# Performance work log

Measured on AMD Instinct MI355X. Metric: run time of the kernel, lower is better.

The kernel has to match this reference:

```python
import jax, jax.numpy as jnp
import numpy as np

N_GRAPH = 100000
N_CAND = 10
N_TOTAL = N_GRAPH + N_CAND
F_IN = 128
N_TYPES = 10
E = 6400000


def _p(key, shape, scale=0.05):
    return scale * jax.random.normal(key, shape, dtype=jnp.float32)


def setup_inputs() -> dict:
    key = jax.random.key(0)
    ks = jax.random.split(key, 20)
    x = jax.random.normal(ks[0], (N_GRAPH, F_IN), dtype=jnp.float32)
    candidate_set = jax.random.normal(ks[1], (N_CAND, F_IN), dtype=jnp.float32)
    edge_index = jax.random.randint(ks[2], (2, E), 0, N_GRAPH, dtype=jnp.int64)
    candidate_idx = jnp.arange(N_GRAPH, N_TOTAL, dtype=jnp.int64)  # candidate nodes appended last
    return {
        "x": x, "candidate_set": candidate_set,
        "edge_index": edge_index, "candidate_idx": candidate_idx,
        "W1": _p(ks[3], (F_IN, 16)), "b1": jnp.zeros((16,), jnp.float32),
        "W2": _p(ks[4], (16, 24)), "b2": jnp.zeros((24,), jnp.float32),
        "W3": _p(ks[5], (24, 32)), "b3": jnp.zeros((32,), jnp.float32),
        "Ws1": _p(ks[6], (32, 16)), "bs1": jnp.zeros((16,), jnp.float32),
        "Ws2": _p(ks[7], (16, N_TYPES)), "bs2": jnp.zeros((N_TYPES,), jnp.float32),
        "We1": _p(ks[8], (32, 24)), "be1": jnp.zeros((24,), jnp.float32),
        "We2": _p(ks[9], (24, N_TYPES)), "be2": jnp.zeros((N_TYPES,), jnp.float32),
    }


def _gcn(h, src, dst, W, b, n):
    # GCNConv: x' = D^{-1/2}(A+I)D^{-1/2} X W + b (self-loops added)
    h = h @ W
    deg = jax.ops.segment_sum(jnp.ones(src.shape, h.dtype), dst, num_segments=n) + 1.0
    dinv = jax.lax.rsqrt(deg)
    msg = h[src] * (dinv[src] * dinv[dst])[:, None]
    out = jax.ops.segment_sum(msg, dst, num_segments=n)
    out = out + h * (dinv * dinv)[:, None]  # self-loop term
    return out + b


def relu6(x):
    return jnp.clip(x, 0.0, 6.0)


def reference(x, candidate_set, edge_index, candidate_idx,
              W1, b1, W2, b2, W3, b3,
              Ws1, bs1, Ws2, bs2, We1, be1, We2, be2):
    n = N_TOTAL
    src, dst = edge_index[0], edge_index[1]
    h = jnp.concatenate([x, candidate_set], axis=0)  # [n, F_IN]
    h = _gcn(h, src, dst, W1, b1, n)
    h = _gcn(h, src, dst, W2, b2, n)
    h = _gcn(h, src, dst, W3, b3, n)  # [n, 32]

    start_probs = jax.nn.softmax(relu6(h @ Ws1 + bs1) @ Ws2 + bs2, axis=0)  # [n, T]
    mask = jnp.ones_like(start_probs).at[candidate_idx].set(0.0)
    start_probs = start_probs * mask
    start_probs = jnp.where(start_probs == 0.0, 1e-10, start_probs)
    k1, k2 = jax.random.split(jax.random.key(42))
    start_node = jax.random.categorical(k1, jnp.log(start_probs), axis=-1)  # [n]

    combined = jnp.concatenate([h, h[start_node]], axis=0)  # [2n, 32]
    end_probs = jax.nn.softmax(relu6(combined @ We1 + be1) @ We2 + be2, axis=0)  # [2n, T]
    end_probs = end_probs.at[start_node].set(0.0)
    end_probs = jnp.where(end_probs == 0.0, 1e-10, end_probs)
    end_node = jax.random.categorical(k2, jnp.log(end_probs), axis=-1)  # [2n]
    return (start_node, end_node, start_probs, end_probs)
```

## Files before the change

### kernel.cpp

```cpp
#include <hip/hip_runtime.h>
#include <stdint.h>

constexpr int N_GRAPH = 100000;
constexpr int N_CANDS = 10;
constexpr int NT      = N_GRAPH + N_CANDS;
constexpr int F_IN    = 128;
constexpr int NTYPES  = 10;
constexpr int NE      = 6400000;

constexpr int CB_SHIFT = 9;
constexpr int CB       = 1 << CB_SHIFT;
constexpr int NBK2     = (NT + CB - 1) / CB;
constexpr int SB       = 512;
constexpr int NMAT     = NBK2 * SB;
constexpr int NSCAN_B  = NMAT / 256;
constexpr int TMPENT_CAP = NE + NMAT * 15 + 16;

#define RNG_VARIANT 0

typedef float f4v __attribute__((ext_vector_type(4)));

__device__ __forceinline__ void tf2x32(uint32_t k0, uint32_t k1, uint32_t x0, uint32_t x1,
                                       uint32_t& o0, uint32_t& o1) {
  const uint32_t ks2 = k0 ^ k1 ^ 0x1BD11BDAu;
  uint32_t v0 = x0 + k0, v1 = x1 + k1;
#define TFR(r) { v0 += v1; v1 = (v1 << (r)) | (v1 >> (32 - (r))); v1 ^= v0; }
  TFR(13) TFR(15) TFR(26) TFR(6)
  v0 += k1;  v1 += ks2 + 1u;
  TFR(17) TFR(29) TFR(16) TFR(24)
  v0 += ks2; v1 += k0 + 2u;
  TFR(13) TFR(15) TFR(26) TFR(6)
  v0 += k0;  v1 += k1 + 3u;
  TFR(17) TFR(29) TFR(16) TFR(24)
  v0 += k1;  v1 += ks2 + 4u;
  TFR(13) TFR(15) TFR(26) TFR(6)
  v0 += ks2; v1 += k0 + 5u;
#undef TFR
  o0 = v0; o1 = v1;
}

__device__ __forceinline__ void derive_keys(uint32_t& a0, uint32_t& a1,
                                            uint32_t& b0, uint32_t& b1) {
#if RNG_VARIANT == 2
  uint32_t c0, c1, d0, d1;
  tf2x32(0u, 42u, 0u, 2u, c0, c1);
  tf2x32(0u, 42u, 1u, 3u, d0, d1);
  a0 = c0; a1 = d0; b0 = c1; b1 = d1;
#else
  tf2x32(0u, 42u, 0u, 0u, a0, a1);
  tf2x32(0u, 42u, 0u, 1u, b0, b1);
#endif
}

__device__ __forceinline__ uint32_t rng_bits(uint32_t k0, uint32_t k1,
                                             uint32_t idx, uint32_t total) {
#if RNG_VARIANT == 0
  uint32_t o0, o1; tf2x32(k0, k1, 0u, idx, o0, o1); return o0 ^ o1;
#elif RNG_VARIANT == 1
  uint32_t o0, o1; tf2x32(k0, k1, 0u, idx, o0, o1); return o1;
#else
  uint32_t half = total >> 1; uint32_t o0, o1;
  if (idx < half) { tf2x32(k0, k1, idx, idx + half, o0, o1); return o0; }
  tf2x32(k0, k1, idx - half, idx, o0, o1); return o1;
#endif
}

__device__ __forceinline__ double gumbel_from_bits(uint32_t bits) {
  float uf = __uint_as_float((bits >> 9) | 0x3f800000u) - 1.0f;
  uf = fmaxf(1.17549435e-38f, uf + 1.17549435e-38f);
  return -log(-log((double)uf));
}

__device__ __forceinline__ uint32_t encf(float f) {
  uint32_t u = __float_as_uint(f);
  return u ^ ((u & 0x80000000u) ? 0xFFFFFFFFu : 0x80000000u);
}
__device__ __forceinline__ float decf(uint32_t e) {
  uint32_t u = (e & 0x80000000u) ? (e ^ 0x80000000u) : ~e;
  return __uint_as_float(u);
}

__global__ __launch_bounds__(512) void k_bcount(const int* __restrict__ dst,
                                                int* __restrict__ cntmat,
                                                int* __restrict__ cnt) {
  __shared__ int h[NBK2];
  int tid = threadIdx.x, blk = blockIdx.x;
  for (int b = tid; b < NBK2; b += 512) h[b] = 0;
  __syncthreads();
  int per = (NE + SB - 1) / SB;
  int e0 = blk * per, e1 = min(e0 + per, NE);
  for (int e = e0 + tid; e < e1; e += 512) atomicAdd(&h[dst[e] >> CB_SHIFT], 1);
  __syncthreads();
  for (int b = tid; b < NBK2; b += 512) {
    int c = h[b];
    cntmat[b * SB + blk] = (c + 15) & ~15;
    if (c) atomicAdd(&cnt[b], c);
  }
}

__global__ __launch_bounds__(256) void k_s1(int* __restrict__ cmat, int* __restrict__ partial) {
  __shared__ int sm[256];
  int t = blockIdx.x * 256 + threadIdx.x;
  int v = cmat[t];
  sm[threadIdx.x] = v;
  __syncthreads();
  #pragma unroll
  for (int s = 1; s < 256; s <<= 1) {
    int a = (threadIdx.x >= s) ? sm[threadIdx.x - s] : 0;
    __syncthreads();
    sm[threadIdx.x] += a;
    __syncthreads();
  }
  cmat[t] = sm[threadIdx.x] - v;
  if (threadIdx.x == 255) partial[blockIdx.x] = sm[255];
}

__global__ __launch_bounds__(512) void k_s2(int* __restrict__ partial, int* __restrict__ cmat) {
  __shared__ int sm[512];
  int t = threadIdx.x;
  int v = (t < NSCAN_B) ? partial[t] : 0;
  sm[t] = v;
  __syncthreads();
  #pragma unroll
  for (int s = 1; s < 512; s <<= 1) {
    int a = (t >= s) ? sm[t - s] : 0;
    __syncthreads();
    sm[t] += a;
    __syncthreads();
  }
  if (t < NSCAN_B) partial[t] = sm[t] - v;
  if (t == 511) cmat[NMAT] = sm[511];
}

__global__ __launch_bounds__(256) void k_s3(int* __restrict__ cmat, const int* __restrict__ partial) {
  int t = blockIdx.x * 256 + threadIdx.x;
  cmat[t] += partial[blockIdx.x];
}

__global__ __launch_bounds__(256) void k_rowscan(const int* __restrict__ cnt,
                                                 int* __restrict__ rowbase) {
  __shared__ int sm[256];
  int t = threadIdx.x;
  int v = (t < NBK2) ? cnt[t] : 0;
  sm[t] = v;
  __syncthreads();
  #pragma unroll
  for (int s = 1; s < 256; s <<= 1) {
    int a = (t >= s) ? sm[t - s] : 0;
    __syncthreads();
    sm[t] += a;
    __syncthreads();
  }
  if (t < NBK2) rowbase[t] = sm[t] - v;
}

__global__ __launch_bounds__(512) void k_scatter2(const int* __restrict__ src,
                                                  const int* __restrict__ dst,
                                                  const int* __restrict__ cmat,
                                                  uint32_t* __restrict__ tmpent) {
  __shared__ int lcur[NBK2];
  int tid = threadIdx.x, blk = blockIdx.x;
  for (int b = tid; b < NBK2; b += 512) lcur[b] = cmat[b * SB + blk];
  __syncthreads();
  int per = (NE + SB - 1) / SB;
  int e0 = blk * per, e1 = min(e0 + per, NE);
  for (int e = e0 + tid; e < e1; e += 512) {
    int s = src[e], d = dst[e];
    int b = d >> CB_SHIFT;
    int pos = atomicAdd(&lcur[b], 1);
    tmpent[pos] = (uint32_t)s | ((uint32_t)(d & (CB - 1)) << 17);
  }
  __syncthreads();
  for (int b = tid; b < NBK2; b += 512) {
    int p = lcur[b];
    int end = cmat[b * SB + blk + 1];
    for (; p < end; ++p) tmpent[p] = 0xFFFFFFFFu;
  }
}

__global__ __launch_bounds__(512) void k_place(const uint32_t* __restrict__ tmpent,
                                               const int* __restrict__ cmat,
                                               const int* __restrict__ rowbase,
                                               int* __restrict__ rowptr,
                                               float* __restrict__ dinv,
                                               int* __restrict__ col) {
  __shared__ int sdeg[CB];
  __shared__ int sexc[CB];
  __shared__ int sscan[CB];
  int b = blockIdx.x, tid = threadIdx.x;
  sdeg[tid] = 0;
  __syncthreads();
  int r0 = cmat[b * SB], r1 = cmat[(b + 1) * SB];
  for (int e = r0 + tid; e < r1; e += 512) {
    uint32_t v = tmpent[e];
    if (v != 0xFFFFFFFFu) atomicAdd(&sdeg[v >> 17], 1);
  }
  __syncthreads();
  int d = sdeg[tid];
  sscan[tid] = d;
  __syncthreads();
  #pragma unroll
  for (int s = 1; s < CB; s <<= 1) {
    int v = (tid >= s) ? sscan[tid - s] : 0;
    __syncthreads();
    sscan[tid] += v;
    __syncthreads();
  }
  int rb = rowbase[b];
  int incl = rb + sscan[tid];
  sexc[tid] = incl - d;
  int i = b * CB + tid;
  if (i < NT) {
    rowptr[i + 1] = incl;
    dinv[i] = (float)(1.0 / sqrt((double)(d + 1)));
  }
  if (b == 0 && tid == 0) rowptr[0] = 0;
  __syncthreads();
  for (int e = r0 + tid; e < r1; e += 512) {
    uint32_t v = tmpent[e];
    if (v != 0xFFFFFFFFu) {
      int pos = atomicAdd(&sexc[v >> 17], 1);
      col[pos] = (int)(v & 0x1FFFFu);
    }
  }
}

__global__ __launch_bounds__(256) void k_mm1(const float* __restrict__ x, const float* __restrict__ cand,
                                             const float* __restrict__ W, const float* __restrict__ dinv,
                                             float* __restrict__ zs0) {
  int gid = blockIdx.x * 256 + threadIdx.x;
  if (gid >= NT * 4) return;
  int i = gid >> 2, f4 = gid & 3;
  const float* hr = (i < N_GRAPH) ? (x + (size_t)i * F_IN)
                                  : (cand + (size_t)(i - N_GRAPH) * F_IN);
  const float4* h4 = reinterpret_cast<const float4*>(hr);
  const float4* W4 = reinterpret_cast<const float4*>(W);
  double a0 = 0.0, a1 = 0.0, a2 = 0.0, a3 = 0.0;
  #pragma unroll 8
  for (int q = 0; q < 32; ++q) {
    float4 hv = h4[q];
    float4 w0 = W4[(4 * q + 0) * 4 + f4];
    float4 w1 = W4[(4 * q + 1) * 4 + f4];
    float4 w2 = W4[(4 * q + 2) * 4 + f4];
    float4 w3 = W4[(4 * q + 3) * 4 + f4];
    a0 += (double)hv.x * w0.x + (double)hv.y * w1.x + (double)hv.z * w2.x + (double)hv.w * w3.x;
    a1 += (double)hv.x * w0.y + (double)hv.y * w1.y + (double)hv.z * w2.y + (double)hv.w * w3.y;
    a2 += (double)hv.x * w0.z + (double)hv.y * w1.z + (double)hv.z * w2.z + (double)hv.w * w3.z;
    a3 += (double)hv.x * w0.w + (double)hv.y * w1.w + (double)hv.z * w2.w + (double)hv.w * w3.w;
  }
  double di = (double)dinv[i];
  float4 o;
  o.x = (float)(a0 * di); o.y = (float)(a1 * di);
  o.z = (float)(a2 * di); o.w = (float)(a3 * di);
  reinterpret_cast<float4*>(zs0)[(size_t)i * 4 + f4] = o;
}

template <bool SQ, bool WITHW, int R>
__global__ __launch_bounds__(8 * R) void k_prop3(const int* __restrict__ rowptr,
                                                 const int* __restrict__ col,
                                                 const float* __restrict__ zin,
                                                 const float* __restrict__ win,
                                                 const float* __restrict__ dinv,
                                                 float* __restrict__ zout,
                                                 float* __restrict__ wout,
                                                 float* __restrict__ wsout) {
  int i = blockIdx.x * R + threadIdx.y;
  if (i >= NT) return;
  int fx = threadIdx.x & 3;
  int es = threadIdx.x >> 2;
  const float4* z4 = reinterpret_cast<const float4*>(zin);
  int e0 = rowptr[i], e1 = rowptr[i + 1];
  int ngrp = (e1 - e0) >> 2;
  double a0 = 0.0, a1 = 0.0, a2 = 0.0, a3 = 0.0, wa = 0.0;
  const bool dow = WITHW && (fx == 0);
  for (int gq = es; gq < ngrp; gq += 2) {
    int e = e0 + (gq << 2);
    int c0 = __builtin_nontemporal_load(col + e);
    int c1 = __builtin_nontemporal_load(col + e + 1);
    int c2 = __builtin_nontemporal_load(col + e + 2);
    int c3 = __builtin_nontemporal_load(col + e + 3);
    float4 v0 = z4[(size_t)c0 * 4 + fx];
    float4 v1 = z4[(size_t)c1 * 4 + fx];
    float4 v2 = z4[(size_t)c2 * 4 + fx];
    float4 v3 = z4[(size_t)c3 * 4 + fx];
    if (dow)
      wa += (double)win[c0] + (double)win[c1] + (double)win[c2] + (double)win[c3];
    a0 += (double)v0.x + (double)v1.x + (double)v2.x + (double)v3.x;
    a1 += (double)v0.y + (double)v1.y + (double)v2.y + (double)v3.y;
    a2 += (double)v0.z + (double)v1.z + (double)v2.z + (double)v3.z;
    a3 += (double)v0.w + (double)v1.w + (double)v2.w + (double)v3.w;
  }
  if (es == (ngrp & 1)) {
    for (int e = e0 + (ngrp << 2); e < e1; ++e) {
      int c = __builtin_nontemporal_load(col + e);
      float4 v = z4[(size_t)c * 4 + fx];
      if (dow) wa += (double)win[c];
      a0 += (double)v.x; a1 += (double)v.y; a2 += (double)v.z; a3 += (double)v.w;
    }
  }
  a0 += __shfl_xor(a0, 4);
  a1 += __shfl_xor(a1, 4);
  a2 += __shfl_xor(a2, 4);
  a3 += __shfl_xor(a3, 4);
  if (WITHW) wa += __shfl_xor(wa, 4);
  if (es == 0) {
    float4 s = z4[(size_t)i * 4 + fx];
    a0 += (double)s.x; a1 += (double)s.y; a2 += (double)s.z; a3 += (double)s.w;
    double di = (double)dinv[i];
    double sc = SQ ? di * di : di;
    float4 o;
    o.x = (float)(sc * a0); o.y = (float)(sc * a1);
    o.z = (float)(sc * a2); o.w = (float)(sc * a3);
    reinterpret_cast<float4*>(zout)[(size_t)i * 4 + fx] = o;
    if (dow) {
      wa += (double)win[i];
      double w = di * wa;
      wout[i]  = (float)w;
      wsout[i] = (float)(di * w);
    }
  }
}

__global__ __launch_bounds__(512) void k_small(const float* __restrict__ W2, const float* __restrict__ b2p,
                                               const float* __restrict__ W3, const float* __restrict__ b1p,
                                               double* __restrict__ M, double* __restrict__ u,
                                               double* __restrict__ v) {
  __shared__ double t[24];
  int tid = threadIdx.x;
  if (tid < 24) {
    double a = 0.0;
    for (int k = 0; k < 16; ++k) a += (double)b1p[k] * (double)W2[k * 24 + tid];
    t[tid] = a;
  }
  if (tid >= 32 && tid < 64) {
    int o = tid - 32;
    double a = 0.0;
    for (int j = 0; j < 24; ++j) a += (double)b2p[j] * (double)W3[j * 32 + o];
    v[o] = a;
  }
  __syncthreads();
  if (tid < 32) {
    double a = 0.0;
    for (int j = 0; j < 24; ++j) a += t[j] * (double)W3[j * 32 + tid];
    u[tid] = a;
  }
  {
    int k = tid >> 5, o = tid & 31;
    double a = 0.0;
    for (int j = 0; j < 24; ++j) a += (double)W2[k * 24 + j] * (double)W3[j * 32 + o];
    M[tid] = a;
  }
}

__global__ __launch_bounds__(256) void k_epi(const float* __restrict__ z3, const float* __restrict__ w1,
                                             const float* __restrict__ w2,
                                             const double* __restrict__ M, const double* __restrict__ u,
                                             const double* __restrict__ v, const float* __restrict__ b3,
                                             float* __restrict__ H) {
  int gid = blockIdx.x * 256 + threadIdx.x;
  if (gid >= NT * 32) return;
  int i = gid >> 5, o = gid & 31;
  const float* zr = z3 + (size_t)i * 16;
  double acc = (double)b3[o] + (double)w2[i] * u[o] + (double)w1[i] * v[o];
  #pragma unroll
  for (int k = 0; k < 16; ++k) acc += (double)zr[k] * M[k * 32 + o];
  H[gid] = (float)acc;
}

template <int HID>
__global__ __launch_bounds__(256) void k_head(const float* __restrict__ H, const int* __restrict__ sn,
                                              int nrows,
                                              const float* __restrict__ Wa, const float* __restrict__ ba,
                                              const float* __restrict__ Wb, const float* __restrict__ bb,
                                              float* __restrict__ logits) {
  int i = blockIdx.x * 256 + threadIdx.x;
  if (i >= nrows) return;
  int row = (i < NT) ? i : sn[i - NT];
  const float* hr = H + (size_t)row * 32;
  float h[32];
  #pragma unroll
  for (int k = 0; k < 32; ++k) h[k] = hr[k];
  double hid[HID];
  for (int j = 0; j < HID; ++j) {
    double a = (double)ba[j];
    #pragma unroll
    for (int k = 0; k < 32; ++k) a += (double)h[k] * (double)Wa[k * HID + j];
    hid[j] = fmin(fmax(a, 0.0), 6.0);
  }
  for (int t = 0; t < NTYPES; ++t) {
    double l = (double)bb[t];
    #pragma unroll
    for (int j = 0; j < HID; ++j) l += hid[j] * (double)Wb[j * NTYPES + t];
    logits[(size_t)i * NTYPES + t] = (float)l;
  }
}

__global__ __launch_bounds__(256) void k_colmax(const float* __restrict__ L, int nrows,
                                                uint32_t* __restrict__ mb) {
  __shared__ float sm[256][NTYPES];
  float m[NTYPES];
  #pragma unroll
  for (int t = 0; t < NTYPES; ++t) m[t] = -3.402823466e38f;
  for (int r = blockIdx.x * 256 + threadIdx.x; r < nrows; r += gridDim.x * 256) {
    #pragma unroll
    for (int t = 0; t < NTYPES; ++t) m[t] = fmaxf(m[t], L[(size_t)r * NTYPES + t]);
  }
  #pragma unroll
  for (int t = 0; t < NTYPES; ++t) sm[threadIdx.x][t] = m[t];
  __syncthreads();
  for (int s = 128; s > 0; s >>= 1) {
    if (threadIdx.x < s)
      for (int t = 0; t < NTYPES; ++t)
        sm[threadIdx.x][t] = fmaxf(sm[threadIdx.x][t], sm[threadIdx.x + s][t]);
    __syncthreads();
  }
  if (threadIdx.x < NTYPES) atomicMax(&mb[threadIdx.x], encf(sm[0][threadIdx.x]));
}

__global__ __launch_bounds__(256) void k_colsum(const float* __restrict__ L, int nrows,
                                                const uint32_t* __restrict__ mb,
                                                double* __restrict__ sums) {
  __shared__ double sm[256][NTYPES];
  float mx[NTYPES];
  #pragma unroll
  for (int t = 0; t < NTYPES; ++t) mx[t] = decf(mb[t]);
  double s[NTYPES];
  #pragma unroll
  for (int t = 0; t < NTYPES; ++t) s[t] = 0.0;
  for (int r = blockIdx.x * 256 + threadIdx.x; r < nrows; r += gridDim.x * 256) {
    #pragma unroll
    for (int t = 0; t < NTYPES; ++t)
      s[t] += exp((double)L[(size_t)r * NTYPES + t] - (double)mx[t]);
  }
  #pragma unroll
  for (int t = 0; t < NTYPES; ++t) sm[threadIdx.x][t] = s[t];
  __syncthreads();
  for (int st = 128; st > 0; st >>= 1) {
    if (threadIdx.x < st)
      for (int t = 0; t < NTYPES; ++t)
        sm[threadIdx.x][t] += sm[threadIdx.x + st][t];
    __syncthreads();
  }
  if (threadIdx.x < NTYPES) atomicAdd(&sums[threadIdx.x], sm[0][threadIdx.x]);
}

__global__ __launch_bounds__(256) void k_ps_start(const float* __restrict__ L,
                                                  const uint32_t* __restrict__ mb,
                                                  const double* __restrict__ sums,
                                                  float* __restrict__ P,
                                                  float* __restrict__ outSN,
                                                  int* __restrict__ sn,
                                                  int* __restrict__ flags) {
  int i = blockIdx.x * 256 + threadIdx.x;
  if (i >= NT) return;
  uint32_t a0, a1, b0, b1; derive_keys(a0, a1, b0, b1);
  double best = -1e300; int bi = 0;
  #pragma unroll
  for (int t = 0; t < NTYPES; ++t) {
    double p = exp((double)L[(size_t)i * NTYPES + t] - (double)decf(mb[t])) / sums[t];
    float pf = (float)p;
    if (i >= N_GRAPH || pf == 0.0f) pf = 1e-10f;
    P[(size_t)i * NTYPES + t] = pf;
    uint32_t bits = rng_bits(a0, a1, (uint32_t)(i * NTYPES + t), (uint32_t)(NT * NTYPES));
    double v = log((double)pf) + gumbel_from_bits(bits);
    if (v > best) { best = v; bi = t; }
  }
  sn[i] = bi;
  outSN[i] = (float)bi;
  flags[bi] = 1;
}

__global__ __launch_bounds__(256) void k_ps_end(const float* __restrict__ L,
                                                const uint32_t* __restrict__ mb,
                                                const double* __restrict__ sums,
                                                const int* __restrict__ flags,
                                                float* __restrict__ P,
                                                float* __restrict__ outEN) {
  int j = blockIdx.x * 256 + threadIdx.x;
  if (j >= 2 * NT) return;
  uint32_t a0, a1, b0, b1; derive_keys(a0, a1, b0, b1);
  const bool rowmask = (j < NTYPES && flags[j]);
  double best = -1e300; int bi = 0;
  #pragma unroll
  for (int t = 0; t < NTYPES; ++t) {
    double p = exp((double)L[(size_t)j * NTYPES + t] - (double)decf(mb[t])) / sums[t];
    float pf = (float)p;
    if (rowmask || pf == 0.0f) pf = 1e-10f;
    P[(size_t)j * NTYPES + t] = pf;
    uint32_t bits = rng_bits(b0, b1, (uint32_t)(j * NTYPES + t), (uint32_t)(2 * NT * NTYPES));
    double v = log((double)pf) + gumbel_from_bits(bits);
    if (v > best) { best = v; bi = t; }
  }
  outEN[j] = (float)bi;
}

extern "C" void kernel_launch(void* const* d_in, const int* in_sizes, int n_in,
                              void* d_out, int out_size, void* d_ws, size_t ws_size,
                              hipStream_t stream) {
  const float* x    = (const float*)d_in[0];
  const float* cand = (const float*)d_in[1];
  const int*   ei   = (const int*)d_in[2];
  const float* W1 = (const float*)d_in[4];  const float* b1 = (const float*)d_in[5];
  const float* W2 = (const float*)d_in[6];  const float* b2 = (const float*)d_in[7];
  const float* W3 = (const float*)d_in[8];  const float* b3 = (const float*)d_in[9];
  const float* Ws1 = (const float*)d_in[10]; const float* bs1 = (const float*)d_in[11];
  const float* Ws2 = (const float*)d_in[12]; const float* bs2 = (const float*)d_in[13];
  const float* We1 = (const float*)d_in[14]; const float* be1 = (const float*)d_in[15];
  const float* We2 = (const float*)d_in[16]; const float* be2 = (const float*)d_in[17];
  float* out = (float*)d_out;
  float* outSN = out;
  float* outEN = out + NT;
  float* outPS = out + 3 * NT;
  float* outPE = out + 13 * NT;

  char* ws = (char*)d_ws;
  size_t off = 0;
  auto alloc = [&](size_t bytes) -> void* {
    void* p = ws + off;
    off += (bytes + 511) & ~(size_t)511;
    return p;
  };
  float*    dinv    = (float*)alloc((size_t)NT * 4);
  int*      rowptr  = (int*)alloc((size_t)(NT + 1) * 4);
  int*      cnt     = (int*)alloc((size_t)NBK2 * 4);
  int*      rowbase = (int*)alloc((size_t)NBK2 * 4);
  int*      cmat    = (int*)alloc((size_t)(NMAT + 1) * 4);
  int*      partial = (int*)alloc(512 * 4);
  int*      col     = (int*)alloc((size_t)NE * 4);
  char*     ublk    = (char*)alloc((size_t)TMPENT_CAP * 4);
  uint32_t* tmpent  = (uint32_t*)ublk;
  float*    zsA     = (float*)ublk;
  float*    zsB     = (float*)(ublk + (size_t)NT * 16 * 4);
  float*    Ha      = (float*)(ublk + (size_t)NT * 16 * 4 * 2);
  float*    logitsS = (float*)alloc((size_t)NT * NTYPES * 4);
  float*    logitsE = (float*)alloc((size_t)2 * NT * NTYPES * 4);
  float*    w1v     = (float*)alloc((size_t)NT * 4);
  float*    ws1v    = (float*)alloc((size_t)NT * 4);
  float*    w2v     = (float*)alloc((size_t)NT * 4);
  float*    wsd     = (float*)alloc((size_t)NT * 4);
  double*   Md      = (double*)alloc(512 * 8);
  double*   ud      = (double*)alloc(32 * 8);
  double*   vd      = (double*)alloc(32 * 8);
  int*      sn      = (int*)alloc((size_t)NT * 4);
  uint32_t* maxS    = (uint32_t*)alloc(64);
  double*   sumS    = (double*)alloc(128);
  uint32_t* maxE    = (uint32_t*)alloc(64);
  double*   sumE    = (double*)alloc(128);
  int*      flags   = (int*)alloc(64);
  (void)ws_size; (void)in_sizes; (void)n_in; (void)out_size;

  const int* srcA = ei;
  const int* dstA = ei + NE;

  const int B = 256;
  auto blocks = [](long long nthreads) { return (int)((nthreads + 255) / 256); };

  hipMemsetAsync(cnt, 0, (size_t)NBK2 * 4, stream);
  k_bcount<<<SB, 512, 0, stream>>>(dstA, cmat, cnt);
  k_s1<<<NSCAN_B, 256, 0, stream>>>(cmat, partial);
  k_s2<<<1, 512, 0, stream>>>(partial, cmat);
  k_s3<<<NSCAN_B, 256, 0, stream>>>(cmat, partial);
  k_rowscan<<<1, 256, 0, stream>>>(cnt, rowbase);
  k_scatter2<<<SB, 512, 0, stream>>>(srcA, dstA, cmat, tmpent);
  k_place<<<NBK2, 512, 0, stream>>>(tmpent, cmat, rowbase, rowptr, dinv, col);

  k_small<<<1, 512, 0, stream>>>(W2, b2, W3, b1, Md, ud, vd);
  k_mm1<<<blocks((long long)NT * 4), B, 0, stream>>>(x, cand, W1, dinv, zsA);
  const int PR3 = 32, PBLK = (NT + PR3 - 1) / PR3;
  k_prop3<true,  true,  PR3><<<PBLK, dim3(8, PR3), 0, stream>>>(rowptr, col, zsA, dinv, dinv, zsB, w1v, ws1v);
  k_prop3<true,  true,  PR3><<<PBLK, dim3(8, PR3), 0, stream>>>(rowptr, col, zsB, ws1v, dinv, zsA, w2v, wsd);
  k_prop3<false, false, PR3><<<PBLK, dim3(8, PR3), 0, stream>>>(rowptr, col, zsA, nullptr, dinv, zsB, nullptr, nullptr);
  k_epi<<<blocks((long long)NT * 32), B, 0, stream>>>(zsB, w1v, w2v, Md, ud, vd, b3, Ha);

  k_head<16><<<blocks(NT), B, 0, stream>>>(Ha, sn, NT, Ws1, bs1, Ws2, bs2, logitsS);
  hipMemsetAsync(maxS, 0, (size_t)((char*)flags - (char*)maxS) + 512, stream);
  k_colmax<<<512, B, 0, stream>>>(logitsS, NT, maxS);
  k_colsum<<<512, B, 0, stream>>>(logitsS, NT, maxS, sumS);
  k_ps_start<<<blocks(NT), B, 0, stream>>>(logitsS, maxS, sumS, outPS, outSN, sn, flags);

  k_head<24><<<blocks(2 * NT), B, 0, stream>>>(Ha, sn, 2 * NT, We1, be1, We2, be2, logitsE);
  k_colmax<<<512, B, 0, stream>>>(logitsE, 2 * NT, maxE);
  k_colsum<<<512, B, 0, stream>>>(logitsE, 2 * NT, maxE, sumE);
  k_ps_end<<<blocks((long long)2 * NT), B, 0, stream>>>(logitsE, maxE, sumE, flags, outPE, outEN);
}
```

Baseline: 787.5 us.

## Split SpMM gather into two source-half passes for L2 locality

Each row's CSR neighbours are partitioned by whether the source index falls in the lower or upper half of nodes, and each propagation layer runs as two passes, one per half. Partial sums from the first pass go to a double-precision scratch buffer that the second pass reads back and finishes. The aim is that each pass gathers from a feature table half the size, so it fits better in cache and random gathers hit more often. The gather loop is also unrolled to issue eight loads per iteration. In exchange there are extra kernel launches, partial-sum writes and reads, and more shared atomics in CSR placement.

```diff
diff --git a/kernel.cpp b/kernel.cpp
--- a/kernel.cpp
+++ b/kernel.cpp
@@ -16,9 +16,12 @@
 constexpr int NSCAN_B  = NMAT / 256;
 constexpr int TMPENT_CAP = NE + NMAT * 15 + 16;
 
+constexpr int HSPLIT = NT / 2;
+
 #define RNG_VARIANT 0
 
-typedef float f4v __attribute__((ext_vector_type(4)));
+typedef float  f4v __attribute__((ext_vector_type(4)));
+typedef double d2v __attribute__((ext_vector_type(2)));
 
 __device__ __forceinline__ void tf2x32(uint32_t k0, uint32_t k1, uint32_t x0, uint32_t x1,
                                        uint32_t& o0, uint32_t& o1) {
@@ -182,18 +185,26 @@
                                                const int* __restrict__ cmat,
                                                const int* __restrict__ rowbase,
                                                int* __restrict__ rowptr,
+                                               int* __restrict__ rowmid,
                                                float* __restrict__ dinv,
                                                int* __restrict__ col) {
   __shared__ int sdeg[CB];
-  __shared__ int sexc[CB];
+  __shared__ int sdlo[CB];
   __shared__ int sscan[CB];
+  __shared__ int sclo[CB];
+  __shared__ int schi[CB];
   int b = blockIdx.x, tid = threadIdx.x;
   sdeg[tid] = 0;
+  sdlo[tid] = 0;
   __syncthreads();
   int r0 = cmat[b * SB], r1 = cmat[(b + 1) * SB];
   for (int e = r0 + tid; e < r1; e += 512) {
     uint32_t v = tmpent[e];
-    if (v != 0xFFFFFFFFu) atomicAdd(&sdeg[v >> 17], 1);
+    if (v != 0xFFFFFFFFu) {
+      int d = v >> 17;
+      atomicAdd(&sdeg[d], 1);
+      if ((int)(v & 0x1FFFFu) < HSPLIT) atomicAdd(&sdlo[d], 1);
+    }
   }
   __syncthreads();
   int d = sdeg[tid];
@@ -208,10 +219,14 @@
   }
   int rb = rowbase[b];
   int incl = rb + sscan[tid];
-  sexc[tid] = incl - d;
+  int exc  = incl - d;
+  int mid  = exc + sdlo[tid];
+  sclo[tid] = exc;
+  schi[tid] = mid;
   int i = b * CB + tid;
   if (i < NT) {
     rowptr[i + 1] = incl;
+    rowmid[i] = mid;
     dinv[i] = (float)(1.0 / sqrt((double)(d + 1)));
   }
   if (b == 0 && tid == 0) rowptr[0] = 0;
@@ -219,8 +234,10 @@
   for (int e = r0 + tid; e < r1; e += 512) {
     uint32_t v = tmpent[e];
     if (v != 0xFFFFFFFFu) {
-      int pos = atomicAdd(&sexc[v >> 17], 1);
-      col[pos] = (int)(v & 0x1FFFFu);
+      int dd = v >> 17;
+      int s = (int)(v & 0x1FFFFu);
+      int pos = (s < HSPLIT) ? atomicAdd(&sclo[dd], 1) : atomicAdd(&schi[dd], 1);
+      col[pos] = s;
     }
   }
 }
@@ -255,12 +272,15 @@
   reinterpret_cast<float4*>(zs0)[(size_t)i * 4 + f4] = o;
 }
 
-template <bool SQ, bool WITHW, int R>
-__global__ __launch_bounds__(8 * R) void k_prop3(const int* __restrict__ rowptr,
+template <bool SQ, bool WITHW, int PASS, int R>
+__global__ __launch_bounds__(8 * R) void k_prop4(const int* __restrict__ rowptr,
+                                                 const int* __restrict__ rowmid,
                                                  const int* __restrict__ col,
                                                  const float* __restrict__ zin,
                                                  const float* __restrict__ win,
                                                  const float* __restrict__ dinv,
+                                                 double* __restrict__ zpart,
+                                                 double* __restrict__ wpart,
                                                  float* __restrict__ zout,
                                                  float* __restrict__ wout,
                                                  float* __restrict__ wsout) {
@@ -269,11 +289,46 @@
   int fx = threadIdx.x & 3;
   int es = threadIdx.x >> 2;
   const float4* z4 = reinterpret_cast<const float4*>(zin);
-  int e0 = rowptr[i], e1 = rowptr[i + 1];
+  int e0, e1;
+  if (PASS == 0) { e0 = rowptr[i]; e1 = rowmid[i]; }
+  else           { e0 = rowmid[i]; e1 = rowptr[i + 1]; }
   int ngrp = (e1 - e0) >> 2;
   double a0 = 0.0, a1 = 0.0, a2 = 0.0, a3 = 0.0, wa = 0.0;
   const bool dow = WITHW && (fx == 0);
-  for (int gq = es; gq < ngrp; gq += 2) {
+  int gq = es;
+  for (; gq + 4 <= ngrp; gq += 4) {
+    int ea = e0 + (gq << 2);
+    int eb = e0 + ((gq + 2) << 2);
+    int c0 = __builtin_nontemporal_load(col + ea);
+    int c1 = __builtin_nontemporal_load(col + ea + 1);
+    int c2 = __builtin_nontemporal_load(col + ea + 2);
+    int c3 = __builtin_nontemporal_load(col + ea + 3);
+    int c4 = __builtin_nontemporal_load(col + eb);
+    int c5 = __builtin_nontemporal_load(col + eb + 1);
+    int c6 = __builtin_nontemporal_load(col + eb + 2);
+    int c7 = __builtin_nontemporal_load(col + eb + 3);
+    float4 v0 = z4[(size_t)c0 * 4 + fx];
+    float4 v1 = z4[(size_t)c1 * 4 + fx];
+    float4 v2 = z4[(size_t)c2 * 4 + fx];
+    float4 v3 = z4[(size_t)c3 * 4 + fx];
+    float4 v4 = z4[(size_t)c4 * 4 + fx];
+    float4 v5 = z4[(size_t)c5 * 4 + fx];
+    float4 v6 = z4[(size_t)c6 * 4 + fx];
+    float4 v7 = z4[(size_t)c7 * 4 + fx];
+    if (dow) {
+      wa += (double)win[c0] + (double)win[c1] + (double)win[c2] + (double)win[c3];
+      wa += (double)win[c4] + (double)win[c5] + (double)win[c6] + (double)win[c7];
+    }
+    a0 += (double)v0.x + (double)v1.x + (double)v2.x + (double)v3.x;
+    a1 += (double)v0.y + (double)v1.y + (double)v2.y + (double)v3.y;
+    a2 += (double)v0.z + (double)v1.z + (double)v2.z + (double)v3.z;
+    a3 += (double)v0.w + (double)v1.w + (double)v2.w + (double)v3.w;
+    a0 += (double)v4.x + (double)v5.x + (double)v6.x + (double)v7.x;
+    a1 += (double)v4.y + (double)v5.y + (double)v6.y + (double)v7.y;
+    a2 += (double)v4.z + (double)v5.z + (double)v6.z + (double)v7.z;
+    a3 += (double)v4.w + (double)v5.w + (double)v6.w + (double)v7.w;
+  }
+  for (; gq < ngrp; gq += 2) {
     int e = e0 + (gq << 2);
     int c0 = __builtin_nontemporal_load(col + e);
     int c1 = __builtin_nontemporal_load(col + e + 1);
@@ -304,19 +359,32 @@
   a3 += __shfl_xor(a3, 4);
   if (WITHW) wa += __shfl_xor(wa, 4);
   if (es == 0) {
-    float4 s = z4[(size_t)i * 4 + fx];
-    a0 += (double)s.x; a1 += (double)s.y; a2 += (double)s.z; a3 += (double)s.w;
-    double di = (double)dinv[i];
-    double sc = SQ ? di * di : di;
-    float4 o;
-    o.x = (float)(sc * a0); o.y = (float)(sc * a1);
-    o.z = (float)(sc * a2); o.w = (float)(sc * a3);
-    reinterpret_cast<float4*>(zout)[(size_t)i * 4 + fx] = o;
-    if (dow) {
-      wa += (double)win[i];
-      double w = di * wa;
-      wout[i]  = (float)w;
-      wsout[i] = (float)(di * w);
+    d2v* zp = reinterpret_cast<d2v*>(zpart) + (size_t)i * 8 + fx * 2;
+    if (PASS == 0) {
+      d2v p0; p0.x = a0; p0.y = a1;
+      d2v p1; p1.x = a2; p1.y = a3;
+      __builtin_nontemporal_store(p0, zp);
+      __builtin_nontemporal_store(p1, zp + 1);
+      if (dow) wpart[i] = wa;
+    } else {
+      d2v q0 = __builtin_nontemporal_load(zp);
+      d2v q1 = __builtin_nontemporal_load(zp + 1);
+      a0 += q0.x; a1 += q0.y; a2 += q1.x; a3 += q1.y;
+      float4 s = z4[(size_t)i * 4 + fx];
+      a0 += (double)s.x; a1 += (double)s.y; a2 += (double)s.z; a3 += (double)s.w;
+      double di = (double)dinv[i];
+      double sc = SQ ? di * di : di;
+      f4v o;
+      o.x = (float)(sc * a0); o.y = (float)(sc * a1);
+      o.z = (float)(sc * a2); o.w = (float)(sc * a3);
+      __builtin_nontemporal_store(o, reinterpret_cast<f4v*>(zout) + (size_t)i * 4 + fx);
+      if (dow) {
+        wa += wpart[i];
+        wa += (double)win[i];
+        double w = di * wa;
+        wout[i]  = (float)w;
+        wsout[i] = (float)(di * w);
+      }
     }
   }
 }
@@ -522,6 +590,7 @@
   };
   float*    dinv    = (float*)alloc((size_t)NT * 4);
   int*      rowptr  = (int*)alloc((size_t)(NT + 1) * 4);
+  int*      rowmid  = (int*)alloc((size_t)NT * 4);
   int*      cnt     = (int*)alloc((size_t)NBK2 * 4);
   int*      rowbase = (int*)alloc((size_t)NBK2 * 4);
   int*      cmat    = (int*)alloc((size_t)(NMAT + 1) * 4);
@@ -532,6 +601,8 @@
   float*    zsA     = (float*)ublk;
   float*    zsB     = (float*)(ublk + (size_t)NT * 16 * 4);
   float*    Ha      = (float*)(ublk + (size_t)NT * 16 * 4 * 2);
+  double*   zpart   = (double*)Ha;
+  double*   wpart   = (double*)(ublk + (size_t)NT * 16 * 4 * 4);
   float*    logitsS = (float*)alloc((size_t)NT * NTYPES * 4);
   float*    logitsE = (float*)alloc((size_t)2 * NT * NTYPES * 4);
   float*    w1v     = (float*)alloc((size_t)NT * 4);
@@ -562,14 +633,18 @@
   k_s3<<<NSCAN_B, 256, 0, stream>>>(cmat, partial);
   k_rowscan<<<1, 256, 0, stream>>>(cnt, rowbase);
   k_scatter2<<<SB, 512, 0, stream>>>(srcA, dstA, cmat, tmpent);
-  k_place<<<NBK2, 512, 0, stream>>>(tmpent, cmat, rowbase, rowptr, dinv, col);
+  k_place<<<NBK2, 512, 0, stream>>>(tmpent, cmat, rowbase, rowptr, rowmid, dinv, col);
 
   k_small<<<1, 512, 0, stream>>>(W2, b2, W3, b1, Md, ud, vd);
   k_mm1<<<blocks((long long)NT * 4), B, 0, stream>>>(x, cand, W1, dinv, zsA);
   const int PR3 = 32, PBLK = (NT + PR3 - 1) / PR3;
-  k_prop3<true,  true,  PR3><<<PBLK, dim3(8, PR3), 0, stream>>>(rowptr, col, zsA, dinv, dinv, zsB, w1v, ws1v);
-  k_prop3<true,  true,  PR3><<<PBLK, dim3(8, PR3), 0, stream>>>(rowptr, col, zsB, ws1v, dinv, zsA, w2v, wsd);
-  k_prop3<false, false, PR3><<<PBLK, dim3(8, PR3), 0, stream>>>(rowptr, col, zsA, nullptr, dinv, zsB, nullptr, nullptr);
+  dim3 pdim(8, PR3);
+  k_prop4<true,  true,  0, PR3><<<PBLK, pdim, 0, stream>>>(rowptr, rowmid, col, zsA, dinv, dinv, zpart, wpart, nullptr, nullptr, nullptr);
+  k_prop4<true,  true,  1, PR3><<<PBLK, pdim, 0, stream>>>(rowptr, rowmid, col, zsA, dinv, dinv, zpart, wpart, zsB, w1v, ws1v);
+  k_prop4<true,  true,  0, PR3><<<PBLK, pdim, 0, stream>>>(rowptr, rowmid, col, zsB, ws1v, dinv, zpart, wpart, nullptr, nullptr, nullptr);
+  k_prop4<true,  true,  1, PR3><<<PBLK, pdim, 0, stream>>>(rowptr, rowmid, col, zsB, ws1v, dinv, zpart, wpart, zsA, w2v, wsd);
+  k_prop4<false, false, 0, PR3><<<PBLK, pdim, 0, stream>>>(rowptr, rowmid, col, zsA, nullptr, dinv, zpart, wpart, nullptr, nullptr, nullptr);
+  k_prop4<false, false, 1, PR3><<<PBLK, pdim, 0, stream>>>(rowptr, rowmid, col, zsA, nullptr, dinv, zpart, wpart, zsB, nullptr, nullptr);
   k_epi<<<blocks((long long)NT * 32), B, 0, stream>>>(zsB, w1v, w2v, Md, ud, vd, b3, Ha);
 
   k_head<16><<<blocks(NT), B, 0, stream>>>(Ha, sn, NT, Ws1, bs1, Ws2, bs2, logitsS);
```

Measured after the change: 807.7 us. 1.03x slower.
